# Performance work log

Measured on AMD Instinct MI355X. Metric: run time of the kernel, lower is better.

The kernel has to match this reference:

```python
import jax, jax.numpy as jnp
import numpy as np

N = 131072   # queries
M = 8192     # tree nodes
K = 8        # max children per node
DEPTH = 16   # upper bound on traversal depth (complete 8-ary tree of 8192 nodes has depth ~5)
EPS = 1e-6   # torch PairwiseDistance eps (added to the difference)
BIG = 1e9    # finite stand-in for +inf so grads stay clean


def _mlp(x, W1, b1, W2, b2, W3, b3, W4, b4):
    # TransformNetwork: 2 -> 100 -> 100 -> 30 -> 2, ReLU on hidden layers
    h = jax.nn.relu(x @ W1 + b1)
    h = jax.nn.relu(h @ W2 + b2)
    h = jax.nn.relu(h @ W3 + b3)
    return h @ W4 + b4


def setup_inputs() -> dict:
    key = jax.random.key(0)
    ks = jax.random.split(key, 8)
    x = jax.random.normal(ks[0], (N, 2), dtype=jnp.float32)
    node_data = jax.random.normal(ks[1], (M, 2), dtype=jnp.float32)
    rng = np.random.default_rng(0)
    node_classes = jnp.asarray(np.eye(2, dtype=np.float32)[rng.integers(0, 2, M)])
    # complete K-ary tree: parent of node i (i>=1) is (i-1)//K
    ch = np.full((M, K), -1, dtype=np.int32)
    idx = np.arange(1, M)
    ch[(idx - 1) // K, (idx - 1) % K] = idx
    children = jnp.asarray(ch)
    W1 = jax.random.normal(ks[2], (2, 100), dtype=jnp.float32) * 0.7
    W2 = jax.random.normal(ks[3], (100, 100), dtype=jnp.float32) * 0.1
    W3 = jax.random.normal(ks[4], (100, 30), dtype=jnp.float32) * 0.1
    W4 = jax.random.normal(ks[5], (30, 2), dtype=jnp.float32) * 0.18
    b1 = jnp.zeros((100,), jnp.float32)
    b2 = jnp.zeros((100,), jnp.float32)
    b3 = jnp.zeros((30,), jnp.float32)
    b4 = jnp.zeros((2,), jnp.float32)
    return {"x": x, "node_data": node_data, "node_classes": node_classes,
            "children": children, "W1": W1, "b1": b1, "W2": W2, "b2": b2,
            "W3": W3, "b3": b3, "W4": W4, "b4": b4}


def _forward(x, node_data, node_classes, children, W1, b1, W2, b2, W3, b3, W4, b4):
    emb = _mlp(node_data, W1, b1, W2, b2, W3, b3, W4, b4)   # [M,2] transformed node data
    qx = _mlp(x, W1, b1, W2, b2, W3, b3, W4, b4)            # [N,2] transformed queries
    valid = children >= 0                                    # [M,K]
    ch = jnp.where(valid, children, 0)                       # safe gather indices

    def dist(a, b):
        # torch.nn.PairwiseDistance: ||a - b + eps||_2
        return jnp.sqrt(jnp.sum((a - b + EPS) ** 2, axis=-1))

    def traverse(q):
        def step(carry, t):
            cur, prob, done, out = carry
            c_idx = ch[cur]                    # [K]
            c_val = valid[cur]                 # [K]
            c_emb = emb[c_idx]                 # [K,2]
            d0 = dist(emb[cur], q)             # scalar: current node
            dc = jnp.where(c_val, dist(c_emb, q), BIG)          # [K] children (pad -> BIG)
            all_d = jnp.concatenate([d0[None], dc])             # [K+1]
            logp = jax.nn.log_softmax(-all_d)
            max_prob = jnp.max(logp)
            amax = jnp.argmax(logp)
            # quirk in source: first iteration adds max_prob twice (prob = max_prob; prob += max_prob)
            prob_new = prob + max_prob + jnp.where(t == 0, max_prob, 0.0)
            stop = amax == 0
            # prob2: log of softmax(-child-to-current distances)-weighted class mixture
            d2 = jnp.where(c_val, dist(emb[cur], c_emb), BIG)    # [K]
            w = jax.nn.softmax(-d2)                              # pad weights ~0
            mix = w @ (node_classes[c_idx] * c_val[:, None].astype(q.dtype))  # [2]
            prob2 = jnp.log(jnp.maximum(mix, 1e-30))
            has_child = jnp.any(c_val)
            out_stop = jnp.where(has_child, prob_new + prob2, jnp.full((2,), prob_new))
            new_out = jnp.where(done, out, jnp.where(stop, out_stop, out))
            nxt = ch[cur][jnp.maximum(amax - 1, 0)]
            new_cur = jnp.where(done | stop, cur, nxt)
            new_prob = jnp.where(done, prob, prob_new)
            return (new_cur, new_prob, done | stop, new_out), None

        init = (jnp.int32(0), jnp.float32(0.0), jnp.array(False), jnp.zeros((2,), q.dtype))
        (_, _, _, out), _ = jax.lax.scan(step, init, jnp.arange(DEPTH))
        return out

    return jax.vmap(traverse)(qx)   # [N,2]


def reference(x, node_data, node_classes, children, W1, b1, W2, b2, W3, b3, W4, b4):
    return _forward(x, node_data, node_classes, children, W1, b1, W2, b2, W3, b3, W4, b4)
```

## Files before the change

### kernel.cpp

```cpp
#include <hip/hip_runtime.h>
#include <math.h>

#define NQ 131072
#define MN 8192
#define NINT 1024
#define DEPTHT 16
#define EPSD 1e-6f
#define BIGD 1e9f

__global__ __launch_bounds__(256) void transpose_w2(
    const float* __restrict__ W2, float* __restrict__ W2T)
{
    const int i = blockIdx.x * 256 + threadIdx.x;
    if (i < 100 * 100) {
        const int k = i / 100, j = i - k * 100;
        W2T[j * 100 + k] = W2[i];
    }
}

__global__ __launch_bounds__(256, 2) void mlp_kernel(
    const float* __restrict__ x, const float* __restrict__ nd,
    const float* __restrict__ W1, const float* __restrict__ b1,
    const float* __restrict__ W2T, const float* __restrict__ b2,
    const float* __restrict__ W3, const float* __restrict__ b3,
    const float* __restrict__ W4, const float* __restrict__ b4,
    float* __restrict__ outv)
{
    const int r = blockIdx.x * 256 + threadIdx.x;
    const float2 xi = (r < NQ) ? ((const float2*)x)[r]
                               : ((const float2*)nd)[r - NQ];

    float h1[100];
#pragma unroll
    for (int k = 0; k < 100; ++k)
        h1[k] = fmaxf(fmaf(xi.x, W1[k], fmaf(xi.y, W1[100 + k], b1[k])), 0.0f);

    float h3[30];
#pragma unroll
    for (int jj = 0; jj < 30; ++jj) h3[jj] = b3[jj];

    const float* w2 = W2T;
    const float* w3 = W3;
    for (int j = 0; j < 100; ++j) {
        float a0 = 0.0f, a1 = 0.0f;
#pragma unroll
        for (int k = 0; k < 100; k += 2) {
            a0 = fmaf(h1[k],     w2[k],     a0);
            a1 = fmaf(h1[k + 1], w2[k + 1], a1);
        }
        const float h2j = fmaxf(a0 + a1 + b2[j], 0.0f);
#pragma unroll
        for (int jj = 0; jj < 30; ++jj)
            h3[jj] = fmaf(h2j, w3[jj], h3[jj]);
        w2 += 100;
        w3 += 30;
    }

    float o0 = b4[0], o1 = b4[1];
#pragma unroll
    for (int k = 0; k < 30; ++k) {
        const float h = fmaxf(h3[k], 0.0f);
        o0 = fmaf(h, W4[2 * k],     o0);
        o1 = fmaf(h, W4[2 * k + 1], o1);
    }
    ((float2*)outv)[r] = make_float2(o0, o1);
}

__global__ __launch_bounds__(256) void traverse_kernel(
    const float* __restrict__ qx, const float2* __restrict__ emb,
    const float2* __restrict__ cls, float* __restrict__ out)
{
    __shared__ float2 semb[MN];
    __shared__ float2 sp2[NINT];
    {
        const float4* ge = (const float4*)emb;
        float4* se = (float4*)semb;
#pragma unroll
        for (int t = 0; t < 16; ++t)
            se[threadIdx.x + 256 * t] = ge[threadIdx.x + 256 * t];
    }
    __syncthreads();

#pragma unroll
    for (int t = 0; t < 4; ++t) {
        const int i = threadIdx.x + 256 * t;
        const float2 ei = semb[i];
        const int base = 8 * i + 1;
        float d2[8];
        float m2 = BIGD;
#pragma unroll
        for (int j = 0; j < 8; ++j) {
            const int c = base + j;
            const bool v = c < MN;
            const float2 ec = semb[v ? c : 0];
            const float dx = ei.x - ec.x + EPSD;
            const float dy = ei.y - ec.y + EPSD;
            d2[j] = v ? sqrtf(dx * dx + dy * dy) : BIGD;
            m2 = fminf(m2, d2[j]);
        }
        float s2 = 0.0f, mix0 = 0.0f, mix1 = 0.0f;
#pragma unroll
        for (int j = 0; j < 8; ++j) {
            const float w = expf(m2 - d2[j]);
            s2 += w;
            const int c = base + j;
            if (c < MN) {
                const float2 cv = cls[c];
                mix0 = fmaf(w, cv.x, mix0);
                mix1 = fmaf(w, cv.y, mix1);
            }
        }
        mix0 /= s2;
        mix1 /= s2;
        sp2[i] = make_float2(logf(fmaxf(mix0, 1e-30f)),
                             logf(fmaxf(mix1, 1e-30f)));
    }
    __syncthreads();

    const int qi = blockIdx.x * 256 + threadIdx.x;
    const float2 qv = ((const float2*)qx)[qi];

    int cur = 0;
    float d0;
    {
        const float2 e0 = semb[0];
        const float dx = e0.x - qv.x + EPSD;
        const float dy = e0.y - qv.y + EPSD;
        d0 = sqrtf(dx * dx + dy * dy);
    }
    float prob = 0.0f, out0 = 0.0f, out1 = 0.0f;
    bool done = false;

    for (int t = 0; t < DEPTHT; ++t) {
        if (__all(done)) break;
        if (!done) {
            const int base = 8 * cur + 1;

            float dc[8];
#pragma unroll
            for (int j = 0; j < 8; ++j) {
                const int c = base + j;
                const bool v = c < MN;
                const float2 e = semb[v ? c : 0];
                const float dx = e.x - qv.x + EPSD;
                const float dy = e.y - qv.y + EPSD;
                dc[j] = v ? sqrtf(dx * dx + dy * dy) : BIGD;
            }

            float dmin = d0;
            int amax = 0;
#pragma unroll
            for (int j = 0; j < 8; ++j)
                if (dc[j] < dmin) { dmin = dc[j]; amax = j + 1; }

            float s = expf(dmin - d0);
#pragma unroll
            for (int j = 0; j < 8; ++j) s += expf(dmin - dc[j]);
            const float max_prob = -logf(s);
            const float prob_new = prob + max_prob + ((t == 0) ? max_prob : 0.0f);

            if (amax == 0) {
                if (base < MN) {
                    const float2 pp = sp2[cur];
                    out0 = prob_new + pp.x;
                    out1 = prob_new + pp.y;
                } else {
                    out0 = prob_new;
                    out1 = prob_new;
                }
                done = true;
            } else {
                cur  = base + amax - 1;
                d0   = dmin;
                prob = prob_new;
            }
        }
    }

    ((float2*)out)[qi] = make_float2(out0, out1);
}

extern "C" void kernel_launch(void* const* d_in, const int* in_sizes, int n_in,
                              void* d_out, int out_size, void* d_ws, size_t ws_size,
                              hipStream_t stream)
{
    const float* x   = (const float*)d_in[0];
    const float* nd  = (const float*)d_in[1];
    const float* cls = (const float*)d_in[2];
    const float* W1 = (const float*)d_in[4];
    const float* b1 = (const float*)d_in[5];
    const float* W2 = (const float*)d_in[6];
    const float* b2 = (const float*)d_in[7];
    const float* W3 = (const float*)d_in[8];
    const float* b3 = (const float*)d_in[9];
    const float* W4 = (const float*)d_in[10];
    const float* b4 = (const float*)d_in[11];

    float* ws   = (float*)d_ws;
    float* qx   = ws;
    float* embf = ws + 2 * NQ;
    float* w2t  = ws + 2 * (NQ + MN);

    transpose_w2<<<40, 256, 0, stream>>>(W2, w2t);

    mlp_kernel<<<(NQ + MN) / 256, 256, 0, stream>>>(
        x, nd, W1, b1, w2t, b2, W3, b3, W4, b4, qx);

    traverse_kernel<<<NQ / 256, 256, 0, stream>>>(
        qx, (const float2*)embf, (const float2*)cls, (float*)d_out);
}
```

Before: 159.5 us.

## Split MLP layer-2 reduction across two thread halves; precompute node log-mix separately

The MLP kernel now gives each row to two threads. One half computes the first 50 terms of the layer-2 dot products in chunks of 10 outputs and hands partial sums through shared memory to the other half, which finishes them and runs layer 3 and 4. The two halves are software-pipelined with two barriers per stage. This is meant to cut per-thread register pressure so occupancy can rise to 4 blocks, at the cost of extra syncs, shared-memory traffic and idle threads in the first and last stages. The per-node class log-mixture, which every traverse block used to recompute, now comes from a small separate kernel and is loaded into shared memory.

```diff
diff --git a/kernel.cpp b/kernel.cpp
--- a/kernel.cpp
+++ b/kernel.cpp
@@ -18,7 +18,7 @@
     }
 }
 
-__global__ __launch_bounds__(256, 2) void mlp_kernel(
+__global__ __launch_bounds__(256, 4) void mlp_kernel(
     const float* __restrict__ x, const float* __restrict__ nd,
     const float* __restrict__ W1, const float* __restrict__ b1,
     const float* __restrict__ W2T, const float* __restrict__ b2,
@@ -26,49 +26,128 @@
     const float* __restrict__ W4, const float* __restrict__ b4,
     float* __restrict__ outv)
 {
-    const int r = blockIdx.x * 256 + threadIdx.x;
+    __shared__ float part[128][21];
+
+    const int tid  = threadIdx.x;
+    const int half = tid >> 7;
+    const int rl   = tid & 127;
+    const int r    = blockIdx.x * 128 + rl;
+
     const float2 xi = (r < NQ) ? ((const float2*)x)[r]
                                : ((const float2*)nd)[r - NQ];
 
-    float h1[100];
-#pragma unroll
-    for (int k = 0; k < 100; ++k)
-        h1[k] = fmaxf(fmaf(xi.x, W1[k], fmaf(xi.y, W1[100 + k], b1[k])), 0.0f);
+    float h1[50];
+    const int k0 = half * 50;
+#pragma unroll
+    for (int kk = 0; kk < 50; ++kk)
+        h1[kk] = fmaxf(fmaf(xi.x, W1[k0 + kk],
+                       fmaf(xi.y, W1[100 + k0 + kk], b1[k0 + kk])), 0.0f);
 
     float h3[30];
-#pragma unroll
-    for (int jj = 0; jj < 30; ++jj) h3[jj] = b3[jj];
-
-    const float* w2 = W2T;
-    const float* w3 = W3;
-    for (int j = 0; j < 100; ++j) {
-        float a0 = 0.0f, a1 = 0.0f;
-#pragma unroll
-        for (int k = 0; k < 100; k += 2) {
-            a0 = fmaf(h1[k],     w2[k],     a0);
-            a1 = fmaf(h1[k + 1], w2[k + 1], a1);
-        }
-        const float h2j = fmaxf(a0 + a1 + b2[j], 0.0f);
-#pragma unroll
-        for (int jj = 0; jj < 30; ++jj)
-            h3[jj] = fmaf(h2j, w3[jj], h3[jj]);
-        w2 += 100;
-        w3 += 30;
-    }
-
-    float o0 = b4[0], o1 = b4[1];
-#pragma unroll
-    for (int k = 0; k < 30; ++k) {
-        const float h = fmaxf(h3[k], 0.0f);
-        o0 = fmaf(h, W4[2 * k],     o0);
-        o1 = fmaf(h, W4[2 * k + 1], o1);
-    }
-    ((float2*)outv)[r] = make_float2(o0, o1);
+    if (half) {
+#pragma unroll
+        for (int jj = 0; jj < 30; ++jj) h3[jj] = b3[jj];
+    }
+
+    float a0p[10], a1p[10];
+    for (int s = 0; s <= 10; ++s) {
+        if (half == 0 && s < 10) {
+            const int jb = s * 10;
+#pragma unroll
+            for (int j = 0; j < 10; ++j) {
+                const float* w2 = W2T + (jb + j) * 100;
+                float a0 = 0.0f, a1 = 0.0f;
+#pragma unroll
+                for (int k = 0; k < 50; k += 2) {
+                    a0 = fmaf(h1[k],     w2[k],     a0);
+                    a1 = fmaf(h1[k + 1], w2[k + 1], a1);
+                }
+                a0p[j] = a0; a1p[j] = a1;
+            }
+        }
+        if (half == 1 && s > 0) {
+            const int jb = (s - 1) * 10;
+#pragma unroll
+            for (int j = 0; j < 10; ++j) {
+                const float* w2 = W2T + (jb + j) * 100;
+                float a0 = part[rl][j];
+                float a1 = part[rl][10 + j];
+#pragma unroll
+                for (int k = 50; k < 100; k += 2) {
+                    a0 = fmaf(h1[k - 50], w2[k],     a0);
+                    a1 = fmaf(h1[k - 49], w2[k + 1], a1);
+                }
+                const float h2j = fmaxf(a0 + a1 + b2[jb + j], 0.0f);
+                const float* w3 = W3 + (jb + j) * 30;
+#pragma unroll
+                for (int jj = 0; jj < 30; ++jj)
+                    h3[jj] = fmaf(h2j, w3[jj], h3[jj]);
+            }
+        }
+        __syncthreads();
+        if (half == 0 && s < 10) {
+#pragma unroll
+            for (int j = 0; j < 10; ++j) {
+                part[rl][j]      = a0p[j];
+                part[rl][10 + j] = a1p[j];
+            }
+        }
+        __syncthreads();
+    }
+
+    if (half == 1) {
+        float o0 = b4[0], o1 = b4[1];
+#pragma unroll
+        for (int k = 0; k < 30; ++k) {
+            const float h = fmaxf(h3[k], 0.0f);
+            o0 = fmaf(h, W4[2 * k],     o0);
+            o1 = fmaf(h, W4[2 * k + 1], o1);
+        }
+        ((float2*)outv)[r] = make_float2(o0, o1);
+    }
+}
+
+__global__ __launch_bounds__(256) void prob2_kernel(
+    const float2* __restrict__ emb, const float2* __restrict__ cls,
+    float2* __restrict__ p2)
+{
+    const int i = blockIdx.x * 256 + threadIdx.x;
+    const float2 ei = emb[i];
+    const int base = 8 * i + 1;
+
+    float d2[8];
+    float m2 = BIGD;
+#pragma unroll
+    for (int j = 0; j < 8; ++j) {
+        const int c = base + j;
+        const bool v = c < MN;
+        const float2 ec = emb[v ? c : 0];
+        const float dx = ei.x - ec.x + EPSD;
+        const float dy = ei.y - ec.y + EPSD;
+        d2[j] = v ? sqrtf(dx * dx + dy * dy) : BIGD;
+        m2 = fminf(m2, d2[j]);
+    }
+    float s2 = 0.0f, mix0 = 0.0f, mix1 = 0.0f;
+#pragma unroll
+    for (int j = 0; j < 8; ++j) {
+        const float w = expf(m2 - d2[j]);
+        s2 += w;
+        const int c = base + j;
+        if (c < MN) {
+            const float2 cv = cls[c];
+            mix0 = fmaf(w, cv.x, mix0);
+            mix1 = fmaf(w, cv.y, mix1);
+        }
+    }
+    mix0 /= s2;
+    mix1 /= s2;
+    p2[i] = make_float2(logf(fmaxf(mix0, 1e-30f)),
+                        logf(fmaxf(mix1, 1e-30f)));
 }
 
 __global__ __launch_bounds__(256) void traverse_kernel(
     const float* __restrict__ qx, const float2* __restrict__ emb,
-    const float2* __restrict__ cls, float* __restrict__ out)
+    const float2* __restrict__ p2g, float* __restrict__ out)
 {
     __shared__ float2 semb[MN];
     __shared__ float2 sp2[NINT];
@@ -78,42 +157,11 @@
 #pragma unroll
         for (int t = 0; t < 16; ++t)
             se[threadIdx.x + 256 * t] = ge[threadIdx.x + 256 * t];
-    }
-    __syncthreads();
-
-#pragma unroll
-    for (int t = 0; t < 4; ++t) {
-        const int i = threadIdx.x + 256 * t;
-        const float2 ei = semb[i];
-        const int base = 8 * i + 1;
-        float d2[8];
-        float m2 = BIGD;
-#pragma unroll
-        for (int j = 0; j < 8; ++j) {
-            const int c = base + j;
-            const bool v = c < MN;
-            const float2 ec = semb[v ? c : 0];
-            const float dx = ei.x - ec.x + EPSD;
-            const float dy = ei.y - ec.y + EPSD;
-            d2[j] = v ? sqrtf(dx * dx + dy * dy) : BIGD;
-            m2 = fminf(m2, d2[j]);
-        }
-        float s2 = 0.0f, mix0 = 0.0f, mix1 = 0.0f;
-#pragma unroll
-        for (int j = 0; j < 8; ++j) {
-            const float w = expf(m2 - d2[j]);
-            s2 += w;
-            const int c = base + j;
-            if (c < MN) {
-                const float2 cv = cls[c];
-                mix0 = fmaf(w, cv.x, mix0);
-                mix1 = fmaf(w, cv.y, mix1);
-            }
-        }
-        mix0 /= s2;
-        mix1 /= s2;
-        sp2[i] = make_float2(logf(fmaxf(mix0, 1e-30f)),
-                             logf(fmaxf(mix1, 1e-30f)));
+        const float4* gp = (const float4*)p2g;
+        float4* sp = (float4*)sp2;
+#pragma unroll
+        for (int t = 0; t < 2; ++t)
+            sp[threadIdx.x + 256 * t] = gp[threadIdx.x + 256 * t];
     }
     __syncthreads();
 
@@ -199,13 +247,17 @@
     float* ws   = (float*)d_ws;
     float* qx   = ws;
     float* embf = ws + 2 * NQ;
-    float* w2t  = ws + 2 * (NQ + MN);
+    float* p2f  = ws + 2 * (NQ + MN);
+    float* w2t  = p2f + 2 * NINT;
 
     transpose_w2<<<40, 256, 0, stream>>>(W2, w2t);
 
-    mlp_kernel<<<(NQ + MN) / 256, 256, 0, stream>>>(
+    mlp_kernel<<<(NQ + MN) / 128, 256, 0, stream>>>(
         x, nd, W1, b1, w2t, b2, W3, b3, W4, b4, qx);
 
+    prob2_kernel<<<NINT / 256, 256, 0, stream>>>(
+        (const float2*)embf, (const float2*)cls, (float2*)p2f);
+
     traverse_kernel<<<NQ / 256, 256, 0, stream>>>(
-        qx, (const float2*)embf, (const float2*)cls, (float*)d_out);
-}
+        qx, (const float2*)embf, (const float2*)p2f, (float*)d_out);
+}
```

New measurement: 366.0 us. 2.3x slower.

## Stage MLP weights in LDS and hoist per-node prob2 into a separate kernel

Applied to the files above, without the earlier changes.

The MLP kernel now copies W2T and a padded W3 into shared memory per block, so the inner loops read weights from LDS instead of global or scalar memory. The per-block recomputation of the internal-node class-mixture log-probabilities is moved out of every traverse block into a small prob2 kernel that runs once. Each traverse block then loads those 1024 values from global memory. In exchange there is an extra kernel launch, and about 52 KB of LDS per MLP block, which can lower occupancy and turns uniform weight reads into LDS broadcasts.

```diff
diff --git a/kernel.cpp b/kernel.cpp
--- a/kernel.cpp
+++ b/kernel.cpp
@@ -26,7 +26,22 @@
     const float* __restrict__ W4, const float* __restrict__ b4,
     float* __restrict__ outv)
 {
-    const int r = blockIdx.x * 256 + threadIdx.x;
+    __shared__ float sW2[100 * 100];
+    __shared__ float sW3[100 * 32];
+
+    const int tid = threadIdx.x;
+    {
+        const float4* g = (const float4*)W2T;
+        float4* s = (float4*)sW2;
+        for (int i = tid; i < 2500; i += 256) s[i] = g[i];
+        for (int i = tid; i < 3000; i += 256) {
+            const int row = i / 30, col = i - row * 30;
+            sW3[row * 32 + col] = W3[i];
+        }
+    }
+    __syncthreads();
+
+    const int r = blockIdx.x * 256 + tid;
     const float2 xi = (r < NQ) ? ((const float2*)x)[r]
                                : ((const float2*)nd)[r - NQ];
 
@@ -39,9 +54,8 @@
 #pragma unroll
     for (int jj = 0; jj < 30; ++jj) h3[jj] = b3[jj];
 
-    const float* w2 = W2T;
-    const float* w3 = W3;
     for (int j = 0; j < 100; ++j) {
+        const float* w2 = sW2 + j * 100;
         float a0 = 0.0f, a1 = 0.0f;
 #pragma unroll
         for (int k = 0; k < 100; k += 2) {
@@ -49,11 +63,10 @@
             a1 = fmaf(h1[k + 1], w2[k + 1], a1);
         }
         const float h2j = fmaxf(a0 + a1 + b2[j], 0.0f);
+        const float* w3 = sW3 + j * 32;
 #pragma unroll
         for (int jj = 0; jj < 30; ++jj)
             h3[jj] = fmaf(h2j, w3[jj], h3[jj]);
-        w2 += 100;
-        w3 += 30;
     }
 
     float o0 = b4[0], o1 = b4[1];
@@ -66,9 +79,47 @@
     ((float2*)outv)[r] = make_float2(o0, o1);
 }
 
+__global__ __launch_bounds__(256) void prob2_kernel(
+    const float2* __restrict__ emb, const float2* __restrict__ cls,
+    float2* __restrict__ p2)
+{
+    const int i = blockIdx.x * 256 + threadIdx.x;
+    const float2 ei = emb[i];
+    const int base = 8 * i + 1;
+
+    float d2[8];
+    float m2 = BIGD;
+#pragma unroll
+    for (int j = 0; j < 8; ++j) {
+        const int c = base + j;
+        const bool v = c < MN;
+        const float2 ec = emb[v ? c : 0];
+        const float dx = ei.x - ec.x + EPSD;
+        const float dy = ei.y - ec.y + EPSD;
+        d2[j] = v ? sqrtf(dx * dx + dy * dy) : BIGD;
+        m2 = fminf(m2, d2[j]);
+    }
+    float s2 = 0.0f, mix0 = 0.0f, mix1 = 0.0f;
+#pragma unroll
+    for (int j = 0; j < 8; ++j) {
+        const float w = expf(m2 - d2[j]);
+        s2 += w;
+        const int c = base + j;
+        if (c < MN) {
+            const float2 cv = cls[c];
+            mix0 = fmaf(w, cv.x, mix0);
+            mix1 = fmaf(w, cv.y, mix1);
+        }
+    }
+    mix0 /= s2;
+    mix1 /= s2;
+    p2[i] = make_float2(logf(fmaxf(mix0, 1e-30f)),
+                        logf(fmaxf(mix1, 1e-30f)));
+}
+
 __global__ __launch_bounds__(256) void traverse_kernel(
     const float* __restrict__ qx, const float2* __restrict__ emb,
-    const float2* __restrict__ cls, float* __restrict__ out)
+    const float2* __restrict__ p2g, float* __restrict__ out)
 {
     __shared__ float2 semb[MN];
     __shared__ float2 sp2[NINT];
@@ -78,42 +129,11 @@
 #pragma unroll
         for (int t = 0; t < 16; ++t)
             se[threadIdx.x + 256 * t] = ge[threadIdx.x + 256 * t];
-    }
-    __syncthreads();
-
-#pragma unroll
-    for (int t = 0; t < 4; ++t) {
-        const int i = threadIdx.x + 256 * t;
-        const float2 ei = semb[i];
-        const int base = 8 * i + 1;
-        float d2[8];
-        float m2 = BIGD;
-#pragma unroll
-        for (int j = 0; j < 8; ++j) {
-            const int c = base + j;
-            const bool v = c < MN;
-            const float2 ec = semb[v ? c : 0];
-            const float dx = ei.x - ec.x + EPSD;
-            const float dy = ei.y - ec.y + EPSD;
-            d2[j] = v ? sqrtf(dx * dx + dy * dy) : BIGD;
-            m2 = fminf(m2, d2[j]);
-        }
-        float s2 = 0.0f, mix0 = 0.0f, mix1 = 0.0f;
-#pragma unroll
-        for (int j = 0; j < 8; ++j) {
-            const float w = expf(m2 - d2[j]);
-            s2 += w;
-            const int c = base + j;
-            if (c < MN) {
-                const float2 cv = cls[c];
-                mix0 = fmaf(w, cv.x, mix0);
-                mix1 = fmaf(w, cv.y, mix1);
-            }
-        }
-        mix0 /= s2;
-        mix1 /= s2;
-        sp2[i] = make_float2(logf(fmaxf(mix0, 1e-30f)),
-                             logf(fmaxf(mix1, 1e-30f)));
+        const float4* gp = (const float4*)p2g;
+        float4* sp = (float4*)sp2;
+#pragma unroll
+        for (int t = 0; t < 2; ++t)
+            sp[threadIdx.x + 256 * t] = gp[threadIdx.x + 256 * t];
     }
     __syncthreads();
 
@@ -199,13 +219,17 @@
     float* ws   = (float*)d_ws;
     float* qx   = ws;
     float* embf = ws + 2 * NQ;
-    float* w2t  = ws + 2 * (NQ + MN);
+    float* p2f  = ws + 2 * (NQ + MN);
+    float* w2t  = p2f + 2 * NINT;
 
     transpose_w2<<<40, 256, 0, stream>>>(W2, w2t);
 
     mlp_kernel<<<(NQ + MN) / 256, 256, 0, stream>>>(
         x, nd, W1, b1, w2t, b2, W3, b3, W4, b4, qx);
 
+    prob2_kernel<<<NINT / 256, 256, 0, stream>>>(
+        (const float2*)embf, (const float2*)cls, (float2*)p2f);
+
     traverse_kernel<<<NQ / 256, 256, 0, stream>>>(
-        qx, (const float2*)embf, (const float2*)cls, (float*)d_out);
-}
+        qx, (const float2*)embf, (const float2*)p2f, (float*)d_out);
+}
```

Result: slower. 178.5 us (+11.9%).
